# Kernel optimization log

Hardware: AMD Instinct MI355X
Metric: run time of the kernel (lower is better)

Reference implementation:

```python
import jax, jax.numpy as jnp
import numpy as np
from jax import lax

C = 256
HEADS = 8
AREA = 4
MLP_DIM = int(1.2 * C)  # 307


def _conv1x1(x, w, s, b):
    # x: [B,C,H,W], w: [O,C], s,b: [O]  (Conv2d 1x1 bias=False + folded BN)
    y = jnp.einsum('bchw,oc->bohw', x, w)
    return y * s[None, :, None, None] + b[None, :, None, None]


def _dwconv3x3(x, w, s, b):
    # depthwise 3x3, groups=C; w: [C,1,3,3]
    y = lax.conv_general_dilated(x, w, (1, 1), ((1, 1), (1, 1)),
                                 feature_group_count=x.shape[1],
                                 dimension_numbers=('NCHW', 'OIHW', 'NCHW'))
    return y * s[None, :, None, None] + b[None, :, None, None]


def setup_inputs() -> dict:
    key = jax.random.key(0)
    ks = jax.random.split(key, 8)
    B, H, W = 2, 64, 64
    x = jax.random.normal(ks[0], (B, C, H, W), dtype=jnp.float32)
    std = 0.02
    w_qk = jax.random.normal(ks[1], (2 * C, C), dtype=jnp.float32) * std
    w_v = jax.random.normal(ks[2], (C, C), dtype=jnp.float32) * std
    w_pe = jax.random.normal(ks[3], (C, 1, 3, 3), dtype=jnp.float32) * std
    w_proj = jax.random.normal(ks[4], (C, C), dtype=jnp.float32) * std
    w_m1 = jax.random.normal(ks[5], (MLP_DIM, C), dtype=jnp.float32) * std
    w_m2 = jax.random.normal(ks[6], (C, MLP_DIM), dtype=jnp.float32) * std
    ones = lambda n: jnp.ones((n,), jnp.float32)
    zeros = lambda n: jnp.zeros((n,), jnp.float32)
    return {
        'x': x,
        'w_qk': w_qk, 's_qk': ones(2 * C), 'b_qk': zeros(2 * C),
        'w_v': w_v, 's_v': ones(C), 'b_v': zeros(C),
        'w_pe': w_pe, 's_pe': ones(C), 'b_pe': zeros(C),
        'w_proj': w_proj, 's_proj': ones(C), 'b_proj': zeros(C),
        'w_m1': w_m1, 's_m1': ones(MLP_DIM), 'b_m1': zeros(MLP_DIM),
        'w_m2': w_m2, 's_m2': ones(C), 'b_m2': zeros(C),
    }


def _block(x, w_qk, s_qk, b_qk, w_v, s_v, b_v, w_pe, s_pe, b_pe,
           w_proj, s_proj, b_proj, w_m1, s_m1, b_m1, w_m2, s_m2, b_m2):
    B, Cc, H, W = x.shape
    N = H * W
    hd = Cc // HEADS
    scale = hd ** -0.5

    # --- AreaAttention ---
    qk = _conv1x1(x, w_qk, s_qk, b_qk).reshape(B, 2 * Cc, N)
    v4 = _conv1x1(x, w_v, s_v, b_v)                 # [B,C,H,W]
    pe = _dwconv3x3(v4, w_pe, s_pe, b_pe)           # positional encoding
    v = v4.reshape(B, Cc, N)

    # area split (row-major reshape, identical to torch contiguous reshape)
    Ba, Na = B * AREA, N // AREA
    qk = qk.reshape(Ba, 2 * Cc, Na)
    v = v.reshape(Ba, Cc, Na)
    q, k = qk[:, :Cc], qk[:, Cc:]
    q = q.reshape(Ba, HEADS, hd, Na)
    k = k.reshape(Ba, HEADS, hd, Na)
    v = v.reshape(Ba, HEADS, hd, Na)

    attn = jnp.einsum('bhdn,bhdm->bhnm', q, k) * scale  # [Ba,H,Na,Na]
    attn = jax.nn.softmax(attn, axis=-1)
    out = jnp.einsum('bhdm,bhnm->bhdn', v, attn)         # [Ba,H,hd,Na]

    out = out.reshape(B, Cc, N).reshape(B, Cc, H, W)
    attn_out = _conv1x1(out + pe, w_proj, s_proj, b_proj)

    x1 = x + attn_out  # add=True (shortcut and in_c==out_c)

    # --- conv2 MLP: Conv(SiLU) -> Conv(act=False) ---
    m = jax.nn.silu(_conv1x1(x1, w_m1, s_m1, b_m1))
    m = _conv1x1(m, w_m2, s_m2, b_m2)
    return x1 + m


def reference(x, w_qk, s_qk, b_qk, w_v, s_v, b_v, w_pe, s_pe, b_pe,
              w_proj, s_proj, b_proj, w_m1, s_m1, b_m1, w_m2, s_m2, b_m2):
    return _block(x, w_qk, s_qk, b_qk, w_v, s_v, b_v, w_pe, s_pe, b_pe,
                  w_proj, s_proj, b_proj, w_m1, s_m1, b_m1, w_m2, s_m2, b_m2)
```

## Files before the change

kernel.cpp:

```cpp
#include <hip/hip_runtime.h>

typedef __attribute__((ext_vector_type(8))) short s8v;
typedef __attribute__((ext_vector_type(4))) float f4v;

#define QSC (0.17677669529663687f * 1.4426950408889634f)

__device__ __forceinline__ unsigned short f2bf(float x) {
    unsigned u = __float_as_uint(x);
    return (unsigned short)((u + 0x7fffu + ((u >> 16) & 1u)) >> 16);
}
__device__ __forceinline__ float bf2f(unsigned short h) {
    return __uint_as_float(((unsigned)h) << 16);
}
__device__ __forceinline__ unsigned trunc2(float a, float b) {
    return (__float_as_uint(b) & 0xffff0000u) | (__float_as_uint(a) >> 16);
}

__global__ __launch_bounds__(256) void wconv_kernel(
    const float* __restrict__ wqk, const float* __restrict__ sqk, const float* __restrict__ bqk,
    const float* __restrict__ wv,  const float* __restrict__ sv,  const float* __restrict__ bv,
    const float* __restrict__ wprj, const float* __restrict__ sprj,
    const float* __restrict__ wm1, const float* __restrict__ sm1, const float* __restrict__ bm1,
    const float* __restrict__ wm2, const float* __restrict__ sm2,
    const float* __restrict__ wpe9,
    unsigned short* __restrict__ Wqkv, unsigned short* __restrict__ Wp,
    unsigned short* __restrict__ Wm1,  unsigned short* __restrict__ Wm2,
    float* __restrict__ bpad, float* __restrict__ bqv, float* __restrict__ wpeT)
{
    int i = blockIdx.x * 256 + threadIdx.x;
    if (i < 196608) {
        int o = i >> 8, c = i & 255;
        float w;
        if (o < 512) { float f = ((o & 127) < 64) ? QSC : 1.f; w = wqk[i] * sqk[o] * f; }
        else          w = wv[(o - 512) * 256 + c] * sv[o - 512];
        Wqkv[i] = f2bf(w);
    } else if (i < 262144) {
        int j = i - 196608; int o = j >> 8; Wp[j] = f2bf(wprj[j] * sprj[o]);
    } else if (i < 360448) {
        int j = i - 262144; int o = j >> 8, c = j & 255;
        Wm1[j] = (o < 307) ? f2bf(wm1[o * 256 + c] * sm1[o]) : (unsigned short)0;
    } else if (i < 458752) {
        int j = i - 360448; int o = j / 384, c = j - o * 384;
        Wm2[j] = (c < 307) ? f2bf(wm2[o * 307 + c] * sm2[o]) : (unsigned short)0;
    } else if (i < 459136) {
        int j = i - 458752; bpad[j] = (j < 307) ? bm1[j] : 0.f;
    } else if (i < 459904) {
        int j = i - 459136;
        bqv[j] = (j < 512) ? (bqk[j] * (((j & 127) < 64) ? QSC : 1.f)) : bv[j - 512];
    } else if (i < 462208) {
        int j = i - 459904; int k = j >> 8, c = j & 255;
        wpeT[j] = wpe9[c * 9 + k];
    }
}

__global__ __launch_bounds__(256) void mmqkv_kernel(
    const float* __restrict__ X, const unsigned short* __restrict__ Wb,
    const float* __restrict__ bi,
    unsigned short* __restrict__ qP, unsigned short* __restrict__ kP,
    unsigned short* __restrict__ vC, unsigned short* __restrict__ vT)
{
    __shared__ unsigned short Ap[64][40];
    __shared__ unsigned short Wt[128][40];
    const int tid = threadIdx.x, lane = tid & 63, wv = tid >> 6;
    const int lo4 = lane & 15, quad = lane >> 4;
    const int p0 = blockIdx.x * 64, o0 = blockIdx.y * 128, bB = blockIdx.z;
    const int ph = (wv & 1) * 32, oh = (wv >> 1) * 64;
    const int c2 = tid & 15, pg = tid >> 4;
    const int oW0 = tid >> 2, oW1 = (tid + 256) >> 2;
    const int cW = (tid & 3) * 8;
    const float* xb = X + (size_t)bB * 256 * 4096;

    f4v acc[4][2];
    #pragma unroll
    for (int i = 0; i < 4; i++)
        #pragma unroll
        for (int j = 0; j < 2; j++)
            acc[i][j] = (f4v){0.f, 0.f, 0.f, 0.f};

    float4 fa = *(const float4*)&xb[(size_t)(2 * c2) * 4096 + p0 + pg * 4];
    float4 fb = *(const float4*)&xb[(size_t)(2 * c2 + 1) * 4096 + p0 + pg * 4];
    uint4 wReg0 = *(const uint4*)(Wb + (size_t)(o0 + oW0) * 256 + cW);
    uint4 wReg1 = *(const uint4*)(Wb + (size_t)(o0 + oW1) * 256 + cW);

    for (int kc = 0; kc < 8; kc++) {
        __syncthreads();
        {
            float av[4] = {fa.x, fa.y, fa.z, fa.w};
            float bv2[4] = {fb.x, fb.y, fb.z, fb.w};
            #pragma unroll
            for (int i = 0; i < 4; i++)
                *(unsigned*)&Ap[pg * 4 + i][2 * c2] =
                    (unsigned)f2bf(av[i]) | ((unsigned)f2bf(bv2[i]) << 16);
        }
        *(uint4*)&Wt[oW0][cW] = wReg0;
        *(uint4*)&Wt[oW1][cW] = wReg1;
        __syncthreads();
        if (kc < 7) {
            int k1 = (kc + 1) * 32;
            fa = *(const float4*)&xb[(size_t)(k1 + 2 * c2) * 4096 + p0 + pg * 4];
            fb = *(const float4*)&xb[(size_t)(k1 + 2 * c2 + 1) * 4096 + p0 + pg * 4];
            wReg0 = *(const uint4*)(Wb + (size_t)(o0 + oW0) * 256 + k1 + cW);
            wReg1 = *(const uint4*)(Wb + (size_t)(o0 + oW1) * 256 + k1 + cW);
        }
        s8v af[4], bx[2];
        #pragma unroll
        for (int of = 0; of < 4; of++)
            af[of] = *(const s8v*)&Wt[oh + of * 16 + lo4][quad * 8];
        #pragma unroll
        for (int pf = 0; pf < 2; pf++)
            bx[pf] = *(const s8v*)&Ap[ph + pf * 16 + lo4][quad * 8];
        #pragma unroll
        for (int of = 0; of < 4; of++)
            #pragma unroll
            for (int pf = 0; pf < 2; pf++)
                acc[of][pf] = __builtin_amdgcn_mfma_f32_16x16x32_bf16(af[of], bx[pf], acc[of][pf], 0, 0, 0);
    }
    #pragma unroll
    for (int of = 0; of < 4; of++) {
        int ob = o0 + oh + of * 16 + quad * 4;
        float4 bb = *(const float4*)&bi[ob];
        float bbv[4] = {bb.x, bb.y, bb.z, bb.w};
        #pragma unroll
        for (int pf = 0; pf < 2; pf++) {
            int p = p0 + ph + pf * 16 + lo4;
            unsigned short b4[4];
            #pragma unroll
            for (int r = 0; r < 4; r++) b4[r] = f2bf(acc[of][pf][r] + bbv[r]);
            if (ob < 512) {
                int gg = ob >> 7, rr = ob & 127;
                int hh = (rr & 63) >> 3, j0 = rr & 7;
                unsigned short* dst = (rr >= 64) ? kP : qP;
                *(ushort4*)&dst[((((size_t)(bB * 4 + gg)) * 8 + hh) * 1024 + (p & 1023)) * 32
                                + (p >> 10) * 8 + j0] = *(ushort4*)b4;
            } else {
                *(ushort4*)&vC[((size_t)(bB * 4096 + p)) * 256 + (ob - 512)] = *(ushort4*)b4;
                #pragma unroll
                for (int r = 0; r < 4; r++)
                    vT[((size_t)(bB * 256 + ob - 512 + r)) * 4096 + p] = b4[r];
            }
        }
    }
}

__global__ __launch_bounds__(256) void attn_kernel(
    const unsigned short* __restrict__ qP, const unsigned short* __restrict__ kP,
    const unsigned short* __restrict__ vT,
    unsigned short* __restrict__ Opart, float* __restrict__ Lpart)
{
    __shared__ unsigned short Pq[4][2][32][64];
    const int tid = threadIdx.x;
    const int w = tid >> 6, lane = tid & 63;
    const int lo4 = lane & 15, quad = lane >> 4;
    const int swz = (lo4 & 7) << 4;
    const int n0 = blockIdx.z * 128;
    const int h = blockIdx.y;
    const int z = blockIdx.x;
    const int ba = z >> 1, spl = z & 1;
    const int bB = ba >> 2, g = ba & 3;
    const int mbase = spl * 512;

    const unsigned short* qb = qP + (((size_t)(bB * 4) + g) * 8 + h) * 32768;
    const unsigned short* kb = kP + (((size_t)(bB * 4) + g) * 8 + h) * 32768;

    s8v qf[2];
    #pragma unroll
    for (int qc = 0; qc < 2; qc++)
        qf[qc] = *(const s8v*)(qb + (size_t)(n0 + w * 32 + qc * 16 + lo4) * 32 + quad * 8);
    const int dd0 = lo4, dd1 = 16 + lo4;
    const unsigned short* vb0 = vT + ((size_t)(bB * 256 + g * 64 + h * 8 + (dd0 & 7))) * 4096 + (dd0 >> 3) * 1024 + mbase + quad * 8;
    const unsigned short* vb1 = vT + ((size_t)(bB * 256 + g * 64 + h * 8 + (dd1 & 7))) * 4096 + (dd1 >> 3) * 1024 + mbase + quad * 8;

    f4v oacc[2][2], Lacc[2];
    #pragma unroll
    for (int i = 0; i < 2; i++) {
        Lacc[i] = (f4v){0.f, 0.f, 0.f, 0.f};
        #pragma unroll
        for (int j = 0; j < 2; j++)
            oacc[i][j] = (f4v){0.f, 0.f, 0.f, 0.f};
    }
    s8v ones;
    #pragma unroll
    for (int j = 0; j < 8; j++) ones[j] = (short)0x3F80;

    s8v kf[4], vCur[2][2];
    #pragma unroll
    for (int mf = 0; mf < 4; mf++)
        kf[mf] = *(const s8v*)(kb + (size_t)(mbase + mf * 16 + lo4) * 32 + quad * 8);

    #pragma unroll
    for (int sc = 0; sc < 8; sc++) {
        s8v vNew[2][2];
        #pragma unroll
        for (int mc = 0; mc < 2; mc++) {
            vNew[mc][0] = *(const s8v*)(vb0 + sc * 64 + mc * 32);
            vNew[mc][1] = *(const s8v*)(vb1 + sc * 64 + mc * 32);
        }
        s8v kfn[4];
        if (sc < 7) {
            #pragma unroll
            for (int mf = 0; mf < 4; mf++)
                kfn[mf] = *(const s8v*)(kb + (size_t)(mbase + (sc + 1) * 64 + mf * 16 + lo4) * 32 + quad * 8);
        }
        f4v sT[4][2];
        __builtin_amdgcn_s_setprio(1);
        #pragma unroll
        for (int mf = 0; mf < 4; mf++)
            #pragma unroll
            for (int qc = 0; qc < 2; qc++)
                sT[mf][qc] = __builtin_amdgcn_mfma_f32_16x16x32_bf16(kf[mf], qf[qc], (f4v){0.f, 0.f, 0.f, 0.f}, 0, 0, 0);
        __builtin_amdgcn_s_setprio(0);
        #pragma unroll
        for (int qc = 0; qc < 2; qc++) {
            char* prow = (char*)&Pq[w][sc & 1][qc * 16 + lo4][0];
            #pragma unroll
            for (int mf = 0; mf < 4; mf++) {
                float p0v = __builtin_amdgcn_exp2f(sT[mf][qc][0]);
                float p1v = __builtin_amdgcn_exp2f(sT[mf][qc][1]);
                float p2v = __builtin_amdgcn_exp2f(sT[mf][qc][2]);
                float p3v = __builtin_amdgcn_exp2f(sT[mf][qc][3]);
                uint2 pk;
                pk.x = trunc2(p0v, p1v);
                pk.y = trunc2(p2v, p3v);
                *(uint2*)(prow + ((mf * 32 + quad * 8) ^ swz)) = pk;
            }
        }
        if (sc > 0) {
            #pragma unroll
            for (int mc = 0; mc < 2; mc++) {
                s8v pfr[2];
                #pragma unroll
                for (int qc = 0; qc < 2; qc++)
                    pfr[qc] = *(const s8v*)((const char*)&Pq[w][(sc - 1) & 1][qc * 16 + lo4][0] + ((mc * 64 + quad * 16) ^ swz));
                __builtin_amdgcn_s_setprio(1);
                #pragma unroll
                for (int df = 0; df < 2; df++)
                    #pragma unroll
                    for (int qc = 0; qc < 2; qc++)
                        oacc[df][qc] = __builtin_amdgcn_mfma_f32_16x16x32_bf16(vCur[mc][df], pfr[qc], oacc[df][qc], 0, 0, 0);
                #pragma unroll
                for (int qc = 0; qc < 2; qc++)
                    Lacc[qc] = __builtin_amdgcn_mfma_f32_16x16x32_bf16(ones, pfr[qc], Lacc[qc], 0, 0, 0);
                __builtin_amdgcn_s_setprio(0);
            }
        }
        if (sc < 7) {
            #pragma unroll
            for (int mf = 0; mf < 4; mf++) kf[mf] = kfn[mf];
        }
        #pragma unroll
        for (int mc = 0; mc < 2; mc++) {
            vCur[mc][0] = vNew[mc][0];
            vCur[mc][1] = vNew[mc][1];
        }
    }
    #pragma unroll
    for (int mc = 0; mc < 2; mc++) {
        s8v pfr[2];
        #pragma unroll
        for (int qc = 0; qc < 2; qc++)
            pfr[qc] = *(const s8v*)((const char*)&Pq[w][1][qc * 16 + lo4][0] + ((mc * 64 + quad * 16) ^ swz));
        __builtin_amdgcn_s_setprio(1);
        #pragma unroll
        for (int df = 0; df < 2; df++)
            #pragma unroll
            for (int qc = 0; qc < 2; qc++)
                oacc[df][qc] = __builtin_amdgcn_mfma_f32_16x16x32_bf16(vCur[mc][df], pfr[qc], oacc[df][qc], 0, 0, 0);
        #pragma unroll
        for (int qc = 0; qc < 2; qc++)
            Lacc[qc] = __builtin_amdgcn_mfma_f32_16x16x32_bf16(ones, pfr[qc], Lacc[qc], 0, 0, 0);
        __builtin_amdgcn_s_setprio(0);
    }
    if (quad == 0) {
        size_t lb = (((size_t)(spl * 2 + bB) * 4 + g) * 8 + h) * 1024 + n0 + w * 32;
        Lpart[lb + lo4] = Lacc[0][0];
        Lpart[lb + 16 + lo4] = Lacc[1][0];
    }
    #pragma unroll
    for (int qc = 0; qc < 2; qc++)
        #pragma unroll
        for (int df = 0; df < 2; df++) {
            int pb = df * 2 + (quad >> 1);
            uint2 ov;
            ov.x = trunc2(oacc[df][qc][0], oacc[df][qc][1]);
            ov.y = trunc2(oacc[df][qc][2], oacc[df][qc][3]);
            *(uint2*)(Opart + ((size_t)(spl * 2 + bB) * 4096 + pb * 1024 + n0 + w * 32 + qc * 16 + lo4) * 256
                      + g * 64 + h * 8 + (quad & 1) * 4) = ov;
        }
}

__global__ __launch_bounds__(512) void mlp3_kernel(
    const unsigned short* __restrict__ Opart, const float* __restrict__ Lpart,
    const unsigned short* __restrict__ vC, const float* __restrict__ wpeT,
    const float* __restrict__ spe, const float* __restrict__ bpe,
    const float* __restrict__ x,
    const unsigned short* __restrict__ Wp, const float* __restrict__ bp,
    const unsigned short* __restrict__ Wm1, const float* __restrict__ bm1p,
    const unsigned short* __restrict__ Wm2, const float* __restrict__ bm2,
    float* __restrict__ out)
{
    __shared__ unsigned short bufA[16][392];
    __shared__ unsigned short bufX[16][264];
    const int tid = threadIdx.x, lane = tid & 63, wv = tid >> 6;
    const int lo4 = lane & 15, quad = lane >> 4;
    const int p0 = blockIdx.x * 16, bB = blockIdx.y;

    {
        int row = tid >> 5, cg = (tid & 31) * 8;
        int p = p0 + row;
        int g = cg >> 6, h = (cg >> 3) & 7;
        int na = p & 1023;
        float L = 0.f;
        float o[8] = {};
        #pragma unroll
        for (int spl = 0; spl < 2; spl++) {
            L += Lpart[(((size_t)(spl * 2 + bB) * 4 + g) * 8 + h) * 1024 + na];
            uint4 v = *(const uint4*)(Opart + ((size_t)(spl * 2 + bB) * 4096 + p) * 256 + cg);
            unsigned short tmp[8]; *(uint4*)tmp = v;
            #pragma unroll
            for (int j = 0; j < 8; j++) o[j] += bf2f(tmp[j]);
        }
        float inv = 1.f / L;
        int hh = p >> 6, ww = p & 63;
        float pe[8] = {};
        for (int di = -1; di <= 1; di++) {
            int h2 = hh + di;
            if (h2 < 0 || h2 > 63) continue;
            for (int dj = -1; dj <= 1; dj++) {
                int w2 = ww + dj;
                if (w2 < 0 || w2 > 63) continue;
                uint4 vv = *(const uint4*)(vC + ((size_t)(bB * 4096 + h2 * 64 + w2)) * 256 + cg);
                unsigned short tmp[8]; *(uint4*)tmp = vv;
                int k = (di + 1) * 3 + (dj + 1);
                float4 wa = *(const float4*)&wpeT[k * 256 + cg];
                float4 wb = *(const float4*)&wpeT[k * 256 + cg + 4];
                float ww8[8] = {wa.x, wa.y, wa.z, wa.w, wb.x, wb.y, wb.z, wb.w};
                #pragma unroll
                for (int j = 0; j < 8; j++)
                    pe[j] = fmaf(bf2f(tmp[j]), ww8[j], pe[j]);
            }
        }
        float4 sa = *(const float4*)&spe[cg];
        float4 sb = *(const float4*)&spe[cg + 4];
        float4 b0 = *(const float4*)&bpe[cg];
        float4 b1 = *(const float4*)&bpe[cg + 4];
        float sv8[8] = {sa.x, sa.y, sa.z, sa.w, sb.x, sb.y, sb.z, sb.w};
        float bv8[8] = {b0.x, b0.y, b0.z, b0.w, b1.x, b1.y, b1.z, b1.w};
        unsigned short ob8[8];
        #pragma unroll
        for (int j = 0; j < 8; j++)
            ob8[j] = f2bf(o[j] * inv + pe[j] * sv8[j] + bv8[j]);
        *(uint4*)&bufA[row][cg] = *(uint4*)ob8;
    }
    __syncthreads();

    {
        f4v acc[2] = {(f4v){0.f, 0.f, 0.f, 0.f}, (f4v){0.f, 0.f, 0.f, 0.f}};
        for (int kk = 0; kk < 8; kk++) {
            s8v bx = *(const s8v*)&bufA[lo4][kk * 32 + quad * 8];
            #pragma unroll
            for (int of = 0; of < 2; of++) {
                s8v af = *(const s8v*)(Wp + (size_t)(wv * 32 + of * 16 + lo4) * 256 + kk * 32 + quad * 8);
                acc[of] = __builtin_amdgcn_mfma_f32_16x16x32_bf16(af, bx, acc[of], 0, 0, 0);
            }
        }
        #pragma unroll
        for (int of = 0; of < 2; of++) {
            int ob = wv * 32 + of * 16 + quad * 4;
            float4 bb = *(const float4*)&bp[ob];
            float bbv[4] = {bb.x, bb.y, bb.z, bb.w};
            int p = p0 + lo4;
            unsigned short b4[4];
            #pragma unroll
            for (int r = 0; r < 4; r++) {
                float y = acc[of][r] + bbv[r] + x[((size_t)(bB * 256 + ob + r)) * 4096 + p];
                b4[r] = f2bf(y);
            }
            *(ushort4*)&bufX[lo4][ob] = *(ushort4*)b4;
        }
    }
    __syncthreads();

    {
        f4v acc[3] = {(f4v){0.f, 0.f, 0.f, 0.f}, (f4v){0.f, 0.f, 0.f, 0.f}, (f4v){0.f, 0.f, 0.f, 0.f}};
        for (int kk = 0; kk < 8; kk++) {
            s8v bx = *(const s8v*)&bufX[lo4][kk * 32 + quad * 8];
            #pragma unroll
            for (int of = 0; of < 3; of++) {
                s8v af = *(const s8v*)(Wm1 + (size_t)(wv * 48 + of * 16 + lo4) * 256 + kk * 32 + quad * 8);
                acc[of] = __builtin_amdgcn_mfma_f32_16x16x32_bf16(af, bx, acc[of], 0, 0, 0);
            }
        }
        #pragma unroll
        for (int of = 0; of < 3; of++) {
            int ob = wv * 48 + of * 16 + quad * 4;
            float4 bb = *(const float4*)&bm1p[ob];
            float bbv[4] = {bb.x, bb.y, bb.z, bb.w};
            unsigned short b4[4];
            #pragma unroll
            for (int r = 0; r < 4; r++) {
                float y = acc[of][r] + bbv[r];
                y = y / (1.f + __expf(-y));
                b4[r] = f2bf(y);
            }
            *(ushort4*)&bufA[lo4][ob] = *(ushort4*)b4;
        }
    }
    __syncthreads();

    {
        f4v acc[2] = {(f4v){0.f, 0.f, 0.f, 0.f}, (f4v){0.f, 0.f, 0.f, 0.f}};
        for (int kk = 0; kk < 12; kk++) {
            s8v bx = *(const s8v*)&bufA[lo4][kk * 32 + quad * 8];
            #pragma unroll
            for (int of = 0; of < 2; of++) {
                s8v af = *(const s8v*)(Wm2 + (size_t)(wv * 32 + of * 16 + lo4) * 384 + kk * 32 + quad * 8);
                acc[of] = __builtin_amdgcn_mfma_f32_16x16x32_bf16(af, bx, acc[of], 0, 0, 0);
            }
        }
        #pragma unroll
        for (int of = 0; of < 2; of++) {
            int ob = wv * 32 + of * 16 + quad * 4;
            float4 bb = *(const float4*)&bm2[ob];
            float bbv[4] = {bb.x, bb.y, bb.z, bb.w};
            ushort4 x1v = *(const ushort4*)&bufX[lo4][ob];
            unsigned short x1a[4]; *(ushort4*)x1a = x1v;
            #pragma unroll
            for (int r = 0; r < 4; r++) {
                float y = acc[of][r] + bbv[r] + bf2f(x1a[r]);
                out[((size_t)(bB * 256 + ob + r)) * 4096 + p0 + lo4] = y;
            }
        }
    }
}

extern "C" void kernel_launch(void* const* d_in, const int* in_sizes, int n_in,
                              void* d_out, int out_size, void* d_ws, size_t ws_size,
                              hipStream_t stream)
{
    const float* x      = (const float*)d_in[0];
    const float* w_qk   = (const float*)d_in[1];
    const float* s_qk   = (const float*)d_in[2];
    const float* b_qk   = (const float*)d_in[3];
    const float* w_v    = (const float*)d_in[4];
    const float* s_v    = (const float*)d_in[5];
    const float* b_v    = (const float*)d_in[6];
    const float* w_pe   = (const float*)d_in[7];
    const float* s_pe   = (const float*)d_in[8];
    const float* b_pe   = (const float*)d_in[9];
    const float* w_proj = (const float*)d_in[10];
    const float* s_proj = (const float*)d_in[11];
    const float* b_proj = (const float*)d_in[12];
    const float* w_m1   = (const float*)d_in[13];
    const float* s_m1   = (const float*)d_in[14];
    const float* b_m1   = (const float*)d_in[15];
    const float* w_m2   = (const float*)d_in[16];
    const float* s_m2   = (const float*)d_in[17];
    const float* b_m2   = (const float*)d_in[18];
    float* out = (float*)d_out;

    const size_t NA = (size_t)2 * 4096 * 256;
    unsigned short* vC   = (unsigned short*)d_ws;
    unsigned short* qP   = vC + NA;
    unsigned short* kP   = qP + NA;
    unsigned short* Opart = kP + NA;
    float* Lpart = (float*)(Opart + 2 * NA);
    unsigned short* vT   = (unsigned short*)(Lpart + 131072);
    unsigned short* Wqkv = vT + NA;
    unsigned short* Wp   = Wqkv + 196608;
    unsigned short* Wm1  = Wp + 65536;
    unsigned short* Wm2  = Wm1 + 98304;
    float* bpad = (float*)(Wm2 + 98304);
    float* bqv  = bpad + 384;
    float* wpeT = bqv + 768;

    dim3 blk(256);
    wconv_kernel<<<dim3(1806), blk, 0, stream>>>(
        w_qk, s_qk, b_qk, w_v, s_v, b_v, w_proj, s_proj,
        w_m1, s_m1, b_m1, w_m2, s_m2, w_pe,
        Wqkv, Wp, Wm1, Wm2, bpad, bqv, wpeT);

    mmqkv_kernel<<<dim3(64, 6, 2), blk, 0, stream>>>(x, Wqkv, bqv, qP, kP, vC, vT);

    attn_kernel<<<dim3(16, 8, 8), blk, 0, stream>>>(qP, kP, vT, Opart, Lpart);

    mlp3_kernel<<<dim3(256, 2), dim3(512), 0, stream>>>(
        Opart, Lpart, vC, wpeT, s_pe, b_pe,
        x, Wp, b_proj, Wm1, bpad, Wm2, b_m2, out);
}
```

Before: 173.9 us.

## Make QKV GEMM staging per-wave to remove block barriers, read weights directly

The QKV projection kernel now gives each wave its own LDS tile of converted activations, so the two __syncthreads per K-step go away. Weight fragments are loaded straight from global memory into MFMA registers instead of being staged through shared memory. Each wave converts its 32-pixel slice on its own, which duplicates X loads and conversions across the waves that share a pixel half. Weight reads become uncached per-lane global loads that must finish before the MFMAs can issue. There is also no wave-level fence between the LDS writes and reads, which relies on in-order LDS execution within a wave.

```diff
diff --git a/kernel.cpp b/kernel.cpp
--- a/kernel.cpp
+++ b/kernel.cpp
@@ -59,16 +59,15 @@
     unsigned short* __restrict__ qP, unsigned short* __restrict__ kP,
     unsigned short* __restrict__ vC, unsigned short* __restrict__ vT)
 {
-    __shared__ unsigned short Ap[64][40];
-    __shared__ unsigned short Wt[128][40];
+    __shared__ unsigned short Ap[4][32][40];
     const int tid = threadIdx.x, lane = tid & 63, wv = tid >> 6;
     const int lo4 = lane & 15, quad = lane >> 4;
     const int p0 = blockIdx.x * 64, o0 = blockIdx.y * 128, bB = blockIdx.z;
     const int ph = (wv & 1) * 32, oh = (wv >> 1) * 64;
-    const int c2 = tid & 15, pg = tid >> 4;
-    const int oW0 = tid >> 2, oW1 = (tid + 256) >> 2;
-    const int cW = (tid & 3) * 8;
+    const int c2 = lane & 15, pg = lane >> 4;
     const float* xb = X + (size_t)bB * 256 * 4096;
+    const size_t xr0 = (size_t)(2 * c2) * 4096 + p0 + ph + pg * 4;
+    const size_t xr1 = (size_t)(2 * c2 + 1) * 4096 + p0 + ph + pg * 4;
 
     f4v acc[4][2];
     #pragma unroll
@@ -77,38 +76,39 @@
         for (int j = 0; j < 2; j++)
             acc[i][j] = (f4v){0.f, 0.f, 0.f, 0.f};
 
-    float4 fa = *(const float4*)&xb[(size_t)(2 * c2) * 4096 + p0 + pg * 4];
-    float4 fb = *(const float4*)&xb[(size_t)(2 * c2 + 1) * 4096 + p0 + pg * 4];
-    uint4 wReg0 = *(const uint4*)(Wb + (size_t)(o0 + oW0) * 256 + cW);
-    uint4 wReg1 = *(const uint4*)(Wb + (size_t)(o0 + oW1) * 256 + cW);
+    float4 fa0 = *(const float4*)&xb[xr0];
+    float4 fb0 = *(const float4*)&xb[xr1];
+    float4 fa1 = *(const float4*)&xb[xr0 + 16];
+    float4 fb1 = *(const float4*)&xb[xr1 + 16];
 
     for (int kc = 0; kc < 8; kc++) {
-        __syncthreads();
         {
-            float av[4] = {fa.x, fa.y, fa.z, fa.w};
-            float bv2[4] = {fb.x, fb.y, fb.z, fb.w};
-            #pragma unroll
-            for (int i = 0; i < 4; i++)
-                *(unsigned*)&Ap[pg * 4 + i][2 * c2] =
-                    (unsigned)f2bf(av[i]) | ((unsigned)f2bf(bv2[i]) << 16);
-        }
-        *(uint4*)&Wt[oW0][cW] = wReg0;
-        *(uint4*)&Wt[oW1][cW] = wReg1;
-        __syncthreads();
+            float a0[4] = {fa0.x, fa0.y, fa0.z, fa0.w};
+            float b0[4] = {fb0.x, fb0.y, fb0.z, fb0.w};
+            float a1[4] = {fa1.x, fa1.y, fa1.z, fa1.w};
+            float b1[4] = {fb1.x, fb1.y, fb1.z, fb1.w};
+            #pragma unroll
+            for (int i = 0; i < 4; i++) {
+                *(unsigned*)&Ap[wv][pg * 4 + i][2 * c2] =
+                    (unsigned)f2bf(a0[i]) | ((unsigned)f2bf(b0[i]) << 16);
+                *(unsigned*)&Ap[wv][16 + pg * 4 + i][2 * c2] =
+                    (unsigned)f2bf(a1[i]) | ((unsigned)f2bf(b1[i]) << 16);
+            }
+        }
         if (kc < 7) {
-            int k1 = (kc + 1) * 32;
-            fa = *(const float4*)&xb[(size_t)(k1 + 2 * c2) * 4096 + p0 + pg * 4];
-            fb = *(const float4*)&xb[(size_t)(k1 + 2 * c2 + 1) * 4096 + p0 + pg * 4];
-            wReg0 = *(const uint4*)(Wb + (size_t)(o0 + oW0) * 256 + k1 + cW);
-            wReg1 = *(const uint4*)(Wb + (size_t)(o0 + oW1) * 256 + k1 + cW);
+            size_t k1 = (size_t)(kc + 1) * 32 * 4096;
+            fa0 = *(const float4*)&xb[xr0 + k1];
+            fb0 = *(const float4*)&xb[xr1 + k1];
+            fa1 = *(const float4*)&xb[xr0 + k1 + 16];
+            fb1 = *(const float4*)&xb[xr1 + k1 + 16];
         }
         s8v af[4], bx[2];
         #pragma unroll
         for (int of = 0; of < 4; of++)
-            af[of] = *(const s8v*)&Wt[oh + of * 16 + lo4][quad * 8];
+            af[of] = *(const s8v*)(Wb + (size_t)(o0 + oh + of * 16 + lo4) * 256 + kc * 32 + quad * 8);
         #pragma unroll
         for (int pf = 0; pf < 2; pf++)
-            bx[pf] = *(const s8v*)&Ap[ph + pf * 16 + lo4][quad * 8];
+            bx[pf] = *(const s8v*)&Ap[wv][pf * 16 + lo4][quad * 8];
         #pragma unroll
         for (int of = 0; of < 4; of++)
             #pragma unroll
```

After: 186.5 us. 7.2% more time.
